# Optimization experiments

Hardware: AMD Instinct MI355X
Metric: run time of the kernel (lower is better)

Reference implementation:

```python
import jax, jax.numpy as jnp
import numpy as np

H = 4            # heads
C = 64           # per-head dim (= hidden, PyG TransformerConv semantics)
HD = 64          # hidden_dim
L = 2            # num_layers
NT = 2           # node types: 0=task, 1=machine
ET = ((0, 1), (1, 0))  # edge types: (src_nt, dst_nt)
N = 16384        # nodes per type (== max_nodes -> simple pos-enc slice)
E = 262144       # edges per edge type


def _ln(x, g, b):
    mu = x.mean(-1, keepdims=True)
    var = ((x - mu) ** 2).mean(-1, keepdims=True)
    return (x - mu) * jax.lax.rsqrt(var + 1e-5) * g + b


def _tconv(x_src, x_dst, ei, Wq, bq, Wk, bk, Wv, bv, Ws, bs, Wb):
    # PyG TransformerConv: heads=H, out_channels=C, concat=False, beta=True
    n_dst = x_dst.shape[0]
    src, dst = ei[0], ei[1]
    q = (x_dst @ Wq + bq).reshape(-1, H, C)
    k = (x_src @ Wk + bk).reshape(-1, H, C)
    v = (x_src @ Wv + bv).reshape(-1, H, C)
    logits = jnp.einsum('ehc,ehc->eh', q[dst], k[src]) * (1.0 / float(np.sqrt(C)))  # [E,H]
    m = jax.ops.segment_max(logits, dst, num_segments=n_dst)          # [N,H] segment softmax
    ex = jnp.exp(logits - m[dst])
    denom = jax.ops.segment_sum(ex, dst, num_segments=n_dst)
    alpha = ex / denom[dst]                                            # [E,H]
    msg = (alpha[:, :, None] * v[src]).reshape(-1, H * C)              # [E,H*C]
    out = jax.ops.segment_sum(msg, dst, num_segments=n_dst)
    out = out.reshape(n_dst, H, C).mean(axis=1)                        # concat=False -> head mean
    r = x_dst @ Ws + bs                                                # lin_skip
    beta = jax.nn.sigmoid(jnp.concatenate([out, r, out - r], -1) @ Wb) # lin_beta, [N,1]
    return beta * r + (1.0 - beta) * out


def _forward(edge_index, x, W_in, b_in, type_emb, pos, Wq, bq, Wk, bk, Wv, bv,
             Wskip, bskip, Wbeta, ln_g, ln_b, ff_W1, ff_b1, ff_W2, ff_b2, W_out, b_out):
    # input proj + type embedding + positional encoding (num_nodes == max_nodes -> slice)
    h = [x[t] @ W_in[t] + b_in[t] + type_emb[t] + pos[t] for t in range(NT)]
    for l in range(L):
        hn = [jnp.zeros_like(h[0]), jnp.zeros_like(h[1])]
        for e, (s, d) in enumerate(ET):  # HeteroConv, aggr='sum'
            hn[d] = hn[d] + _tconv(h[s], h[d], edge_index[e],
                                   Wq[l, e], bq[l, e], Wk[l, e], bk[l, e],
                                   Wv[l, e], bv[l, e], Wskip[l, e], bskip[l, e], Wbeta[l, e])
        for t in range(NT):
            hr = _ln(h[t] + hn[t], ln_g[l, t], ln_b[l, t])
            ff = jax.nn.gelu(hr @ ff_W1[l, t] + ff_b1[l, t], approximate=False) @ ff_W2[l, t] + ff_b2[l, t]
            h[t] = hr + ff
    return jnp.stack([h[t] @ W_out[t] + b_out[t] for t in range(NT)])  # [NT,N,HD]


def setup_inputs() -> dict:
    key = jax.random.key(0)
    ks = jax.random.split(key, 16)
    w = lambda k, s: 0.02 * jax.random.normal(k, s, jnp.float32)
    NE = len(ET)
    return {
        'x': jax.random.normal(ks[0], (NT, N, HD), jnp.float32),
        'edge_index': jax.random.randint(ks[1], (NE, 2, E), 0, N, jnp.int32),
        'W_in': w(ks[2], (NT, HD, HD)), 'b_in': jnp.zeros((NT, HD), jnp.float32),
        'type_emb': w(ks[3], (NT, HD)),
        'pos': w(ks[4], (NT, N, HD)),
        'Wq': w(ks[5], (L, NE, HD, H * C)), 'bq': jnp.zeros((L, NE, H * C), jnp.float32),
        'Wk': w(ks[6], (L, NE, HD, H * C)), 'bk': jnp.zeros((L, NE, H * C), jnp.float32),
        'Wv': w(ks[7], (L, NE, HD, H * C)), 'bv': jnp.zeros((L, NE, H * C), jnp.float32),
        'Wskip': w(ks[8], (L, NE, HD, HD)), 'bskip': jnp.zeros((L, NE, HD), jnp.float32),
        'Wbeta': w(ks[9], (L, NE, 3 * HD, 1)),
        'ln_g': jnp.ones((L, NT, HD), jnp.float32), 'ln_b': jnp.zeros((L, NT, HD), jnp.float32),
        'ff_W1': w(ks[10], (L, NT, HD, 4 * HD)), 'ff_b1': jnp.zeros((L, NT, 4 * HD), jnp.float32),
        'ff_W2': w(ks[11], (L, NT, 4 * HD, HD)), 'ff_b2': jnp.zeros((L, NT, HD), jnp.float32),
        'W_out': w(ks[12], (NT, HD, HD)), 'b_out': jnp.zeros((NT, HD), jnp.float32),
    }


def reference(x, edge_index, W_in, b_in, type_emb, pos, Wq, bq, Wk, bk, Wv, bv,
              Wskip, bskip, Wbeta, ln_g, ln_b, ff_W1, ff_b1, ff_W2, ff_b2, W_out, b_out):
    return _forward(edge_index, x, W_in, b_in, type_emb, pos, Wq, bq, Wk, bk, Wv, bv,
                    Wskip, bskip, Wbeta, ln_g, ln_b, ff_W1, ff_b1, ff_W2, ff_b2, W_out, b_out)
```

## Files before the change

kernel.cpp:

```cpp
#include <hip/hip_runtime.h>
#include <math.h>

#define NN 16384
#define EE 262144

typedef __bf16 v8bf __attribute__((ext_vector_type(8)));
typedef __bf16 v4bf __attribute__((ext_vector_type(4)));
typedef float  v4f  __attribute__((ext_vector_type(4)));
typedef float  v2f  __attribute__((ext_vector_type(2)));

#define OFF_CNT     0
#define OFF_FILL    (2*NN)
#define OFF_ROWPTR  (4*NN)
#define OFF_COLSRC  98816
#define OFF_H       623104
#define OFF_HN      (OFF_H  + 2*NN*64)
#define OFF_Q       (OFF_HN + 2*NN*64)
#define OFF_KV      (OFF_Q  + 2*NN*128)
#define OFF_R       (OFF_KV + 2*NN*192)

__device__ __forceinline__ float blo(unsigned u) { return __uint_as_float(u << 16); }
__device__ __forceinline__ float bhi(unsigned u) { return __uint_as_float(u & 0xffff0000u); }
__device__ __forceinline__ unsigned short f2b(float f) {
  __bf16 h = (__bf16)f;
  return *(unsigned short*)&h;
}

__global__ void count_kernel(const int* __restrict__ ei, int* __restrict__ cnt) {
  int idx = blockIdx.x * 256 + threadIdx.x;
  if (idx >= 2 * EE) return;
  int et = idx >> 18;
  int j  = idx & (EE - 1);
  int dst = ei[et * 2 * EE + EE + j];
  atomicAdd(&cnt[et * NN + dst], 1);
}

__global__ __launch_bounds__(1024) void scan_kernel(const int* __restrict__ cnt,
                                                    int* __restrict__ rowptr,
                                                    int* __restrict__ fill) {
  int et = blockIdx.x;
  const int* c = cnt + et * NN;
  __shared__ int sums[1024];
  int tid = threadIdx.x;
  int base = tid * 16;
  int loc[16];
  int s = 0;
#pragma unroll
  for (int i = 0; i < 16; ++i) { loc[i] = s; s += c[base + i]; }
  sums[tid] = s;
  __syncthreads();
  for (int off = 1; off < 1024; off <<= 1) {
    int v = 0;
    if (tid >= off) v = sums[tid - off];
    __syncthreads();
    if (tid >= off) sums[tid] += v;
    __syncthreads();
  }
  int ebase = (tid == 0) ? 0 : sums[tid - 1];
  int* rp = rowptr + et * (NN + 1);
  int* fl = fill + et * NN;
#pragma unroll
  for (int i = 0; i < 16; ++i) {
    rp[base + i] = ebase + loc[i];
    fl[base + i] = ebase + loc[i];
  }
  if (tid == 1023) rp[NN] = sums[1023];
}

__global__ void scatter_kernel(const int* __restrict__ ei, int* __restrict__ fill,
                               int* __restrict__ colsrc) {
  int idx = blockIdx.x * 256 + threadIdx.x;
  if (idx >= 2 * EE) return;
  int et = idx >> 18;
  int j  = idx & (EE - 1);
  int src = ei[et * 2 * EE + j];
  int dst = ei[et * 2 * EE + EE + j];
  int pos = atomicAdd(&fill[et * NN + dst], 1);
  colsrc[et * EE + pos] = (et * NN + src) * 768;
}

struct GemmDesc {
  const float *A, *B, *bias, *bias2, *add;
  char* C;
  int K, Ncols, Cld, tile0, ntiles, gelu, otype;
};
struct GemmPack { GemmDesc d[8]; int nd; };

#define LDA 72

__global__ __launch_bounds__(256) void gemm_mfma(GemmPack p) {
  int y = blockIdx.y;
  int di = 0;
  for (int i = 0; i < p.nd; ++i)
    if (y >= p.d[i].tile0 && y < p.d[i].tile0 + p.d[i].ntiles) di = i;
  GemmDesc g = p.d[di];
  const int col0 = (y - g.tile0) * 64;
  const int row0 = blockIdx.x * 128;
  const int tid = threadIdx.x;
  const int w = tid >> 6, lane = tid & 63;
  const int l16 = lane & 15, quad = lane >> 4;

  __shared__ __bf16 As[128 * LDA];
  __shared__ __bf16 Bs[64 * LDA];

  v4f acc[2][4];
#pragma unroll
  for (int rt = 0; rt < 2; ++rt)
#pragma unroll
    for (int ct = 0; ct < 4; ++ct)
#pragma unroll
      for (int r = 0; r < 4; ++r) acc[rt][ct][r] = 0.f;

  for (int kt = 0; kt < g.K; kt += 64) {
#pragma unroll
    for (int it = 0; it < 8; ++it) {
      int fi = it * 256 + tid;
      int grow = fi >> 4;
      int kq = (fi & 15) << 2;
      float4 a = *(const float4*)(g.A + (size_t)(row0 + grow) * g.K + kt + kq);
      v4bf c = { (__bf16)a.x, (__bf16)a.y, (__bf16)a.z, (__bf16)a.w };
      *(v4bf*)&As[grow * LDA + kq] = c;
    }
#pragma unroll
    for (int it = 0; it < 4; ++it) {
      int fi = it * 256 + tid;
      int kk = fi >> 4;
      int nq = (fi & 15) << 2;
      float4 b = *(const float4*)(g.B + (size_t)(kt + kk) * g.Ncols + col0 + nq);
      Bs[(nq + 0) * LDA + kk] = (__bf16)b.x;
      Bs[(nq + 1) * LDA + kk] = (__bf16)b.y;
      Bs[(nq + 2) * LDA + kk] = (__bf16)b.z;
      Bs[(nq + 3) * LDA + kk] = (__bf16)b.w;
    }
    __syncthreads();
#pragma unroll
    for (int ks = 0; ks < 2; ++ks) {
      v8bf a0 = *(v8bf*)&As[(w * 32 + l16) * LDA + ks * 32 + quad * 8];
      v8bf a1 = *(v8bf*)&As[(w * 32 + 16 + l16) * LDA + ks * 32 + quad * 8];
#pragma unroll
      for (int ct = 0; ct < 4; ++ct) {
        v8bf bb = *(v8bf*)&Bs[(ct * 16 + l16) * LDA + ks * 32 + quad * 8];
        acc[0][ct] = __builtin_amdgcn_mfma_f32_16x16x32_bf16(a0, bb, acc[0][ct], 0, 0, 0);
        acc[1][ct] = __builtin_amdgcn_mfma_f32_16x16x32_bf16(a1, bb, acc[1][ct], 0, 0, 0);
      }
    }
    __syncthreads();
  }

  float bias_c[4];
#pragma unroll
  for (int ct = 0; ct < 4; ++ct) {
    int col = col0 + ct * 16 + l16;
    float b = g.bias ? g.bias[col] : 0.f;
    if (g.bias2) b += g.bias2[col];
    bias_c[ct] = b;
  }
#pragma unroll
  for (int rt = 0; rt < 2; ++rt)
#pragma unroll
    for (int r = 0; r < 4; ++r) {
      size_t row = row0 + w * 32 + rt * 16 + quad * 4 + r;
      char* cp = g.C + row * (size_t)g.Cld;
#pragma unroll
      for (int ct = 0; ct < 4; ++ct) {
        int col = col0 + ct * 16 + l16;
        float v = acc[rt][ct][r] + bias_c[ct];
        if (g.add) v += g.add[row * g.Ncols + col];
        if (g.gelu) v = 0.5f * v * (1.f + erff(v * 0.70710678118654752f));
        if (g.otype == 0)      *(float*)(cp + col * 4) = v;
        else if (g.otype == 1) *(unsigned short*)(cp + col * 2) = f2b(v);
        else {
          unsigned pk = __builtin_amdgcn_cvt_pk_fp8_f32(v, v, 0, false);
          *(unsigned char*)(cp + col) = (unsigned char)(pk & 0xff);
        }
      }
    }
}

struct FFPack {
  const float *HN, *W1, *b1, *W2, *b2;
  float* H;
};

__global__ __launch_bounds__(256) void ff_fused(FFPack p) {
  const int t = blockIdx.y;
  const int row0 = blockIdx.x * 64;
  const int tid = threadIdx.x;
  const int w = tid >> 6, lane = tid & 63;
  const int l16 = lane & 15, quad = lane >> 4;

  const float* A  = p.HN + ((size_t)t * NN) * 64;
  const float* W1 = p.W1 + (size_t)t * 64 * 256;
  const float* b1 = p.b1 + t * 256;
  const float* W2 = p.W2 + (size_t)t * 256 * 64;
  const float* b2 = p.b2 + t * 64;

  __shared__ __bf16 As[64 * LDA];
  __shared__ __bf16 A2[64 * LDA];
  __shared__ __bf16 B1s[64 * LDA];
  __shared__ __bf16 B2s[64 * LDA];

#pragma unroll
  for (int it = 0; it < 4; ++it) {
    int fi = it * 256 + tid;
    int grow = fi >> 4;
    int kq = (fi & 15) << 2;
    float4 a = *(const float4*)(A + (size_t)(row0 + grow) * 64 + kq);
    v4bf c = { (__bf16)a.x, (__bf16)a.y, (__bf16)a.z, (__bf16)a.w };
    *(v4bf*)&As[grow * LDA + kq] = c;
  }

  v4f acc2[4];
#pragma unroll
  for (int ct = 0; ct < 4; ++ct)
#pragma unroll
    for (int r = 0; r < 4; ++r) acc2[ct][r] = 0.f;

  for (int c1 = 0; c1 < 4; ++c1) {
#pragma unroll
    for (int it = 0; it < 4; ++it) {
      int fi = it * 256 + tid;
      int kk = fi >> 4;
      int nq = (fi & 15) << 2;
      float4 b = *(const float4*)(W1 + (size_t)kk * 256 + c1 * 64 + nq);
      B1s[(nq + 0) * LDA + kk] = (__bf16)b.x;
      B1s[(nq + 1) * LDA + kk] = (__bf16)b.y;
      B1s[(nq + 2) * LDA + kk] = (__bf16)b.z;
      B1s[(nq + 3) * LDA + kk] = (__bf16)b.w;
      float4 b2v = *(const float4*)(W2 + (size_t)(c1 * 64 + kk) * 64 + nq);
      B2s[(nq + 0) * LDA + kk] = (__bf16)b2v.x;
      B2s[(nq + 1) * LDA + kk] = (__bf16)b2v.y;
      B2s[(nq + 2) * LDA + kk] = (__bf16)b2v.z;
      B2s[(nq + 3) * LDA + kk] = (__bf16)b2v.w;
    }
    __syncthreads();

    v4f acc1[4];
#pragma unroll
    for (int ct = 0; ct < 4; ++ct)
#pragma unroll
      for (int r = 0; r < 4; ++r) acc1[ct][r] = 0.f;
#pragma unroll
    for (int ks = 0; ks < 2; ++ks) {
      v8bf a = *(v8bf*)&As[(w * 16 + l16) * LDA + ks * 32 + quad * 8];
#pragma unroll
      for (int ct = 0; ct < 4; ++ct) {
        v8bf bb = *(v8bf*)&B1s[(ct * 16 + l16) * LDA + ks * 32 + quad * 8];
        acc1[ct] = __builtin_amdgcn_mfma_f32_16x16x32_bf16(a, bb, acc1[ct], 0, 0, 0);
      }
    }
#pragma unroll
    for (int ct = 0; ct < 4; ++ct) {
      float bb = b1[c1 * 64 + ct * 16 + l16];
#pragma unroll
      for (int r = 0; r < 4; ++r) {
        float v = acc1[ct][r] + bb;
        v = 0.5f * v * (1.f + erff(v * 0.70710678118654752f));
        A2[(w * 16 + quad * 4 + r) * LDA + ct * 16 + l16] = (__bf16)v;
      }
    }
#pragma unroll
    for (int ks = 0; ks < 2; ++ks) {
      v8bf a = *(v8bf*)&A2[(w * 16 + l16) * LDA + ks * 32 + quad * 8];
#pragma unroll
      for (int ct = 0; ct < 4; ++ct) {
        v8bf bb = *(v8bf*)&B2s[(ct * 16 + l16) * LDA + ks * 32 + quad * 8];
        acc2[ct] = __builtin_amdgcn_mfma_f32_16x16x32_bf16(a, bb, acc2[ct], 0, 0, 0);
      }
    }
    __syncthreads();
  }

#pragma unroll
  for (int ct = 0; ct < 4; ++ct) {
    int col = ct * 16 + l16;
    float bb = b2[col];
#pragma unroll
    for (int r = 0; r < 4; ++r) {
      size_t row = (size_t)t * NN + row0 + w * 16 + quad * 4 + r;
      float v = acc2[ct][r] + bb + p.HN[row * 64 + col];
      p.H[row * 64 + col] = v;
    }
  }
}

struct AggPack {
  const unsigned short *Q;
  const char *KV;
  const float *R;
  const float *Wb;
  const float *Hin;
  const float *lng, *lnb;
  float* outHR;
  const int *rowptr;
  const int *colsrc;
};

__global__ __launch_bounds__(256) void agg_kernel(AggPack p) {
  const int et = blockIdx.y, d = 1 - et;
  int wid = __builtin_amdgcn_readfirstlane(threadIdx.x >> 6);
  int lane = threadIdx.x & 63;
  int node = blockIdx.x * 4 + wid;
  int c4 = lane & 15;
  int cb = ((lane >> 4) << 6) + (c4 << 2);

  const int* rp = p.rowptr + et * (NN + 1);
  const int* cs = p.colsrc + et * EE;
  int start = rp[node], end = rp[node + 1];
  int len = end - start;
  int gnode = d * NN + node;

  uint2 qw = *(const uint2*)(p.Q + ((size_t)gnode << 8) + cb);
  float q0 = blo(qw.x) * 0.125f, q1 = bhi(qw.x) * 0.125f;
  float q2 = blo(qw.y) * 0.125f, q3 = bhi(qw.y) * 0.125f;

  int b[5];
#pragma unroll
  for (int i = 0; i <= 4; ++i) b[i] = start + ((len * i) >> 2);
  float dsum[4] = {0.f, 0.f, 0.f, 0.f};
  float acc[4][4];
#pragma unroll
  for (int s4 = 0; s4 < 4; ++s4)
#pragma unroll
    for (int c = 0; c < 4; ++c) acc[s4][c] = 0.f;

  int maxn = (len + 3) >> 2;
  int last = end - 1;
  for (int it = 0; it < maxn; ++it) {
#pragma unroll
    for (int s4 = 0; s4 < 4; ++s4) {
      int j = b[s4] + it;
      bool act = j < b[s4 + 1];
      int jc = act ? j : last;
      int off = cs[jc];
      const char* rowp = p.KV + off;
      unsigned kw = *(const unsigned*)(rowp + cb);
      uint2 vw = *(const uint2*)(rowp + 256 + cb * 2);
      v2f kl = __builtin_amdgcn_cvt_pk_f32_fp8((int)kw, false);
      v2f kh = __builtin_amdgcn_cvt_pk_f32_fp8((int)kw, true);
      float pd = q0 * kl[0] + q1 * kl[1] + q2 * kh[0] + q3 * kh[1];
      pd += __shfl_xor(pd, 1);
      pd += __shfl_xor(pd, 2);
      pd += __shfl_xor(pd, 4);
      pd += __shfl_xor(pd, 8);
      float wgt = act ? __expf(pd) : 0.f;
      dsum[s4] += wgt;
      acc[s4][0] += wgt * blo(vw.x);
      acc[s4][1] += wgt * bhi(vw.x);
      acc[s4][2] += wgt * blo(vw.y);
      acc[s4][3] += wgt * bhi(vw.y);
    }
  }
  float dn = (dsum[0] + dsum[1]) + (dsum[2] + dsum[3]);
  float ax = (acc[0][0] + acc[1][0]) + (acc[2][0] + acc[3][0]);
  float ay = (acc[0][1] + acc[1][1]) + (acc[2][1] + acc[3][1]);
  float az = (acc[0][2] + acc[1][2]) + (acc[2][2] + acc[3][2]);
  float aw = (acc[0][3] + acc[1][3]) + (acc[2][3] + acc[3][3]);

  float inv = (len > 0) ? (0.25f / dn) : 0.f;
  float ox = ax * inv, oy = ay * inv, oz = az * inv, ow = aw * inv;
  ox += __shfl_xor(ox, 16); ox += __shfl_xor(ox, 32);
  oy += __shfl_xor(oy, 16); oy += __shfl_xor(oy, 32);
  oz += __shfl_xor(oz, 16); oz += __shfl_xor(oz, 32);
  ow += __shfl_xor(ow, 16); ow += __shfl_xor(ow, 32);

  int cc = c4 << 2;
  float4 r = *(const float4*)(p.R + (size_t)gnode * 64 + cc);
  const float* wb = p.Wb + et * 192;
  float part = ox * wb[cc] + oy * wb[cc + 1] + oz * wb[cc + 2] + ow * wb[cc + 3]
             + r.x * wb[64 + cc] + r.y * wb[64 + cc + 1]
             + r.z * wb[64 + cc + 2] + r.w * wb[64 + cc + 3]
             + (ox - r.x) * wb[128 + cc] + (oy - r.y) * wb[128 + cc + 1]
             + (oz - r.z) * wb[128 + cc + 2] + (ow - r.w) * wb[128 + cc + 3];
  part += __shfl_xor(part, 1);
  part += __shfl_xor(part, 2);
  part += __shfl_xor(part, 4);
  part += __shfl_xor(part, 8);
  float beta = 1.f / (1.f + __expf(-part));

  float4 hv = *(const float4*)(p.Hin + (size_t)gnode * 64 + cc);
  float yx = hv.x + beta * r.x + (1.f - beta) * ox;
  float yy = hv.y + beta * r.y + (1.f - beta) * oy;
  float yz = hv.z + beta * r.z + (1.f - beta) * oz;
  float yw = hv.w + beta * r.w + (1.f - beta) * ow;
  float sa = yx + yy + yz + yw;
  float sb = yx * yx + yy * yy + yz * yz + yw * yw;
  sa += __shfl_xor(sa, 1); sb += __shfl_xor(sb, 1);
  sa += __shfl_xor(sa, 2); sb += __shfl_xor(sb, 2);
  sa += __shfl_xor(sa, 4); sb += __shfl_xor(sb, 4);
  sa += __shfl_xor(sa, 8); sb += __shfl_xor(sb, 8);
  float mu = sa * (1.f / 64.f);
  float var = sb * (1.f / 64.f) - mu * mu;
  float rs = rsqrtf(var + 1e-5f);
  if (lane < 16) {
    const float* lng = p.lng + d * 64;
    const float* lnb = p.lnb + d * 64;
    float4 gg = *(const float4*)(lng + cc);
    float4 bb = *(const float4*)(lnb + cc);
    float4 res;
    res.x = (yx - mu) * rs * gg.x + bb.x;
    res.y = (yy - mu) * rs * gg.y + bb.y;
    res.z = (yz - mu) * rs * gg.z + bb.z;
    res.w = (yw - mu) * rs * gg.w + bb.w;
    *(float4*)(p.outHR + (size_t)gnode * 64 + cc) = res;
  }
}

static void add_desc(GemmPack& p, int& tiles, const float* A, const float* B,
                     const float* bias, const float* bias2, const float* add,
                     void* C, int K, int Nc, int Cld, int gelu, int otype) {
  GemmDesc& g = p.d[p.nd++];
  g.A = A; g.B = B; g.bias = bias; g.bias2 = bias2; g.add = add; g.C = (char*)C;
  g.K = K; g.Ncols = Nc; g.Cld = Cld; g.tile0 = tiles; g.ntiles = Nc / 64;
  g.gelu = gelu; g.otype = otype;
  tiles += g.ntiles;
}

extern "C" void kernel_launch(void* const* d_in, const int* in_sizes, int n_in,
                              void* d_out, int out_size, void* d_ws, size_t ws_size,
                              hipStream_t stream) {
  const float* x        = (const float*)d_in[0];
  const int*   ei       = (const int*)d_in[1];
  const float* W_in     = (const float*)d_in[2];
  const float* b_in     = (const float*)d_in[3];
  const float* type_emb = (const float*)d_in[4];
  const float* pos      = (const float*)d_in[5];
  const float* Wq       = (const float*)d_in[6];
  const float* bq       = (const float*)d_in[7];
  const float* Wk       = (const float*)d_in[8];
  const float* bk       = (const float*)d_in[9];
  const float* Wv       = (const float*)d_in[10];
  const float* bv       = (const float*)d_in[11];
  const float* Wskip    = (const float*)d_in[12];
  const float* bskip    = (const float*)d_in[13];
  const float* Wbeta    = (const float*)d_in[14];
  const float* ln_g     = (const float*)d_in[15];
  const float* ln_b     = (const float*)d_in[16];
  const float* ff_W1    = (const float*)d_in[17];
  const float* ff_b1    = (const float*)d_in[18];
  const float* ff_W2    = (const float*)d_in[19];
  const float* ff_b2    = (const float*)d_in[20];
  const float* W_out    = (const float*)d_in[21];
  const float* b_out    = (const float*)d_in[22];
  float* out = (float*)d_out;

  int*   wsi = (int*)d_ws;
  float* wsf = (float*)d_ws;
  int* cnt    = wsi + OFF_CNT;
  int* fill   = wsi + OFF_FILL;
  int* rowptr = wsi + OFF_ROWPTR;
  int* colsrc = wsi + OFF_COLSRC;
  float* H  = wsf + OFF_H;
  float* HN = wsf + OFF_HN;
  unsigned short* Qb = (unsigned short*)(wsf + OFF_Q);
  char* KVb = (char*)(wsf + OFF_KV);
  float* Rb = wsf + OFF_R;

  hipMemsetAsync(cnt, 0, 2 * NN * sizeof(int), stream);
  count_kernel<<<dim3(2 * EE / 256), dim3(256), 0, stream>>>(ei, cnt);
  scan_kernel<<<dim3(2), dim3(1024), 0, stream>>>(cnt, rowptr, fill);
  scatter_kernel<<<dim3(2 * EE / 256), dim3(256), 0, stream>>>(ei, fill, colsrc);

  {
    GemmPack p{}; int tiles = 0;
    for (int t = 0; t < 2; ++t)
      add_desc(p, tiles, x + (size_t)t * NN * 64, W_in + t * 64 * 64,
               b_in + t * 64, type_emb + t * 64, pos + (size_t)t * NN * 64,
               H + (size_t)t * NN * 64, 64, 64, 256, 0, 0);
    gemm_mfma<<<dim3(128, tiles), dim3(256), 0, stream>>>(p);
  }

  for (int l = 0; l < 2; ++l) {
    {
      GemmPack p{}; int tiles = 0;
      for (int et = 0; et < 2; ++et) {
        int s = et, d = 1 - et;
        int we = l * 2 + et;
        const float* hs = H + (size_t)s * NN * 64;
        const float* hd = H + (size_t)d * NN * 64;
        add_desc(p, tiles, hd, Wq + (size_t)we * 64 * 256, bq + we * 256,
                 nullptr, nullptr, (char*)Qb + (size_t)d * NN * 512, 64, 256, 512, 0, 1);
        add_desc(p, tiles, hs, Wk + (size_t)we * 64 * 256, bk + we * 256,
                 nullptr, nullptr, KVb + (size_t)s * NN * 768, 64, 256, 768, 0, 2);
        add_desc(p, tiles, hs, Wv + (size_t)we * 64 * 256, bv + we * 256,
                 nullptr, nullptr, KVb + (size_t)s * NN * 768 + 256, 64, 256, 768, 0, 1);
        add_desc(p, tiles, hd, Wskip + (size_t)we * 64 * 64, bskip + we * 64,
                 nullptr, nullptr, Rb + (size_t)d * NN * 64, 64, 64, 256, 0, 0);
      }
      gemm_mfma<<<dim3(128, tiles), dim3(256), 0, stream>>>(p);
    }

    AggPack ap;
    ap.Q = Qb; ap.KV = KVb; ap.R = Rb;
    ap.Wb = Wbeta + l * 2 * 192;
    ap.Hin = H;
    ap.lng = ln_g + l * 128;
    ap.lnb = ln_b + l * 128;
    ap.outHR = HN;
    ap.rowptr = rowptr;
    ap.colsrc = colsrc;
    agg_kernel<<<dim3(NN / 4, 2), dim3(256), 0, stream>>>(ap);

    FFPack fp;
    fp.HN = HN;
    fp.W1 = ff_W1 + (size_t)l * 2 * 64 * 256;
    fp.b1 = ff_b1 + l * 2 * 256;
    fp.W2 = ff_W2 + (size_t)l * 2 * 256 * 64;
    fp.b2 = ff_b2 + l * 2 * 64;
    fp.H  = H;
    ff_fused<<<dim3(NN / 64, 2), dim3(256), 0, stream>>>(fp);
  }

  {
    GemmPack p{}; int tiles = 0;
    for (int t = 0; t < 2; ++t)
      add_desc(p, tiles, H + (size_t)t * NN * 64, W_out + t * 64 * 64,
               b_out + t * 64, nullptr, nullptr,
               out + (size_t)t * NN * 64, 64, 64, 256, 0, 0);
    gemm_mfma<<<dim3(128, tiles), dim3(256), 0, stream>>>(p);
  }
}
```

Baseline: 394.6 us.

## Fuse QKV/skip projections into input-proj and FFN kernels, drop standalone GEMMs

Removes the generic multi-descriptor GEMM kernel. The input projection now produces H in LDS and immediately computes the Q/K/V/skip projections for layer 0. The FFN kernel of layer 0 does the same for layer 1, and the last FFN computes the output projection. This avoids re-reading H from global memory and saves three kernel launches. In exchange, each block runs many sequential weight loads and syncs over 13 column tiles with a single 64-row tile, which may lower parallelism and occupancy per projection.

```diff
diff --git a/kernel.cpp b/kernel.cpp
--- a/kernel.cpp
+++ b/kernel.cpp
@@ -18,6 +18,8 @@
 #define OFF_Q       (OFF_HN + 2*NN*64)
 #define OFF_KV      (OFF_Q  + 2*NN*128)
 #define OFF_R       (OFF_KV + 2*NN*192)
+
+#define LDA 72
 
 __device__ __forceinline__ float blo(unsigned u) { return __uint_as_float(u << 16); }
 __device__ __forceinline__ float bhi(unsigned u) { return __uint_as_float(u & 0xffff0000u); }
@@ -79,107 +81,158 @@
   colsrc[et * EE + pos] = (et * NN + src) * 768;
 }
 
-struct GemmDesc {
-  const float *A, *B, *bias, *bias2, *add;
-  char* C;
-  int K, Ncols, Cld, tile0, ntiles, gelu, otype;
+struct ProjDesc { const float *B, *bias; char* C; int Ncols, Cld, otype; };
+
+__device__ __forceinline__ void project_from_lds(const __bf16* hA, __bf16* Bs,
+                                                 const ProjDesc* pd, int nd,
+                                                 int row0, int tid) {
+  const int w = tid >> 6, lane = tid & 63;
+  const int l16 = lane & 15, quad = lane >> 4;
+  for (int di = 0; di < nd; ++di) {
+    ProjDesc g = pd[di];
+    for (int ct0 = 0; ct0 < (g.Ncols >> 6); ++ct0) {
+      const int col0 = ct0 * 64;
+      __syncthreads();
+#pragma unroll
+      for (int it = 0; it < 4; ++it) {
+        int fi = it * 256 + tid;
+        int kk = fi >> 4;
+        int nq = (fi & 15) << 2;
+        float4 b = *(const float4*)(g.B + (size_t)kk * g.Ncols + col0 + nq);
+        Bs[(nq + 0) * LDA + kk] = (__bf16)b.x;
+        Bs[(nq + 1) * LDA + kk] = (__bf16)b.y;
+        Bs[(nq + 2) * LDA + kk] = (__bf16)b.z;
+        Bs[(nq + 3) * LDA + kk] = (__bf16)b.w;
+      }
+      __syncthreads();
+
+      v4f acc[4];
+#pragma unroll
+      for (int ct = 0; ct < 4; ++ct)
+#pragma unroll
+        for (int r = 0; r < 4; ++r) acc[ct][r] = 0.f;
+#pragma unroll
+      for (int ks = 0; ks < 2; ++ks) {
+        v8bf a = *(v8bf*)&hA[(w * 16 + l16) * LDA + ks * 32 + quad * 8];
+#pragma unroll
+        for (int ct = 0; ct < 4; ++ct) {
+          v8bf bb = *(v8bf*)&Bs[(ct * 16 + l16) * LDA + ks * 32 + quad * 8];
+          acc[ct] = __builtin_amdgcn_mfma_f32_16x16x32_bf16(a, bb, acc[ct], 0, 0, 0);
+        }
+      }
+#pragma unroll
+      for (int ct = 0; ct < 4; ++ct) {
+        int col = col0 + ct * 16 + l16;
+        float bv = g.bias[col];
+#pragma unroll
+        for (int r = 0; r < 4; ++r) {
+          size_t row = row0 + w * 16 + quad * 4 + r;
+          char* cp = g.C + row * (size_t)g.Cld;
+          float v = acc[ct][r] + bv;
+          if (g.otype == 0)      *(float*)(cp + col * 4) = v;
+          else if (g.otype == 1) *(unsigned short*)(cp + col * 2) = f2b(v);
+          else {
+            unsigned pk = __builtin_amdgcn_cvt_pk_fp8_f32(v, v, 0, false);
+            *(unsigned char*)(cp + col) = (unsigned char)(pk & 0xff);
+          }
+        }
+      }
+    }
+  }
+}
+
+struct InQkvPack {
+  const float *x, *Win, *bin, *temb, *pos;
+  const float *Wq, *bq, *Wk, *bk, *Wv, *bv, *Ws, *bs;
+  float* H;
+  unsigned short* Qb;
+  char* KVb;
+  float* Rb;
 };
-struct GemmPack { GemmDesc d[8]; int nd; };
-
-#define LDA 72
-
-__global__ __launch_bounds__(256) void gemm_mfma(GemmPack p) {
-  int y = blockIdx.y;
-  int di = 0;
-  for (int i = 0; i < p.nd; ++i)
-    if (y >= p.d[i].tile0 && y < p.d[i].tile0 + p.d[i].ntiles) di = i;
-  GemmDesc g = p.d[di];
-  const int col0 = (y - g.tile0) * 64;
-  const int row0 = blockIdx.x * 128;
+
+__global__ __launch_bounds__(256) void in_qkv(InQkvPack p) {
+  const int t = blockIdx.y;
+  const int row0 = blockIdx.x * 64;
   const int tid = threadIdx.x;
   const int w = tid >> 6, lane = tid & 63;
   const int l16 = lane & 15, quad = lane >> 4;
 
-  __shared__ __bf16 As[128 * LDA];
+  __shared__ __bf16 As[64 * LDA];
   __shared__ __bf16 Bs[64 * LDA];
 
-  v4f acc[2][4];
-#pragma unroll
-  for (int rt = 0; rt < 2; ++rt)
-#pragma unroll
-    for (int ct = 0; ct < 4; ++ct)
-#pragma unroll
-      for (int r = 0; r < 4; ++r) acc[rt][ct][r] = 0.f;
-
-  for (int kt = 0; kt < g.K; kt += 64) {
-#pragma unroll
-    for (int it = 0; it < 8; ++it) {
-      int fi = it * 256 + tid;
-      int grow = fi >> 4;
-      int kq = (fi & 15) << 2;
-      float4 a = *(const float4*)(g.A + (size_t)(row0 + grow) * g.K + kt + kq);
-      v4bf c = { (__bf16)a.x, (__bf16)a.y, (__bf16)a.z, (__bf16)a.w };
-      *(v4bf*)&As[grow * LDA + kq] = c;
-    }
-#pragma unroll
-    for (int it = 0; it < 4; ++it) {
-      int fi = it * 256 + tid;
-      int kk = fi >> 4;
-      int nq = (fi & 15) << 2;
-      float4 b = *(const float4*)(g.B + (size_t)(kt + kk) * g.Ncols + col0 + nq);
-      Bs[(nq + 0) * LDA + kk] = (__bf16)b.x;
-      Bs[(nq + 1) * LDA + kk] = (__bf16)b.y;
-      Bs[(nq + 2) * LDA + kk] = (__bf16)b.z;
-      Bs[(nq + 3) * LDA + kk] = (__bf16)b.w;
-    }
-    __syncthreads();
-#pragma unroll
-    for (int ks = 0; ks < 2; ++ks) {
-      v8bf a0 = *(v8bf*)&As[(w * 32 + l16) * LDA + ks * 32 + quad * 8];
-      v8bf a1 = *(v8bf*)&As[(w * 32 + 16 + l16) * LDA + ks * 32 + quad * 8];
-#pragma unroll
-      for (int ct = 0; ct < 4; ++ct) {
-        v8bf bb = *(v8bf*)&Bs[(ct * 16 + l16) * LDA + ks * 32 + quad * 8];
-        acc[0][ct] = __builtin_amdgcn_mfma_f32_16x16x32_bf16(a0, bb, acc[0][ct], 0, 0, 0);
-        acc[1][ct] = __builtin_amdgcn_mfma_f32_16x16x32_bf16(a1, bb, acc[1][ct], 0, 0, 0);
-      }
-    }
-    __syncthreads();
-  }
-
-  float bias_c[4];
+  const float* xs = p.x + ((size_t)t * NN) * 64;
+  const float* Win = p.Win + (size_t)t * 64 * 64;
+
+#pragma unroll
+  for (int it = 0; it < 4; ++it) {
+    int fi = it * 256 + tid;
+    int grow = fi >> 4;
+    int kq = (fi & 15) << 2;
+    float4 a = *(const float4*)(xs + (size_t)(row0 + grow) * 64 + kq);
+    v4bf c = { (__bf16)a.x, (__bf16)a.y, (__bf16)a.z, (__bf16)a.w };
+    *(v4bf*)&As[grow * LDA + kq] = c;
+    int kk = grow, nq = kq;
+    float4 b = *(const float4*)(Win + (size_t)kk * 64 + nq);
+    Bs[(nq + 0) * LDA + kk] = (__bf16)b.x;
+    Bs[(nq + 1) * LDA + kk] = (__bf16)b.y;
+    Bs[(nq + 2) * LDA + kk] = (__bf16)b.z;
+    Bs[(nq + 3) * LDA + kk] = (__bf16)b.w;
+  }
+  __syncthreads();
+
+  v4f acc[4];
+#pragma unroll
+  for (int ct = 0; ct < 4; ++ct)
+#pragma unroll
+    for (int r = 0; r < 4; ++r) acc[ct][r] = 0.f;
+#pragma unroll
+  for (int ks = 0; ks < 2; ++ks) {
+    v8bf a = *(v8bf*)&As[(w * 16 + l16) * LDA + ks * 32 + quad * 8];
+#pragma unroll
+    for (int ct = 0; ct < 4; ++ct) {
+      v8bf bb = *(v8bf*)&Bs[(ct * 16 + l16) * LDA + ks * 32 + quad * 8];
+      acc[ct] = __builtin_amdgcn_mfma_f32_16x16x32_bf16(a, bb, acc[ct], 0, 0, 0);
+    }
+  }
+
+  const float* bin = p.bin + t * 64;
+  const float* temb = p.temb + t * 64;
+  const float* pos = p.pos + ((size_t)t * NN) * 64;
 #pragma unroll
   for (int ct = 0; ct < 4; ++ct) {
-    int col = col0 + ct * 16 + l16;
-    float b = g.bias ? g.bias[col] : 0.f;
-    if (g.bias2) b += g.bias2[col];
-    bias_c[ct] = b;
-  }
-#pragma unroll
-  for (int rt = 0; rt < 2; ++rt)
+    int col = ct * 16 + l16;
+    float bb = bin[col] + temb[col];
 #pragma unroll
     for (int r = 0; r < 4; ++r) {
-      size_t row = row0 + w * 32 + rt * 16 + quad * 4 + r;
-      char* cp = g.C + row * (size_t)g.Cld;
-#pragma unroll
-      for (int ct = 0; ct < 4; ++ct) {
-        int col = col0 + ct * 16 + l16;
-        float v = acc[rt][ct][r] + bias_c[ct];
-        if (g.add) v += g.add[row * g.Ncols + col];
-        if (g.gelu) v = 0.5f * v * (1.f + erff(v * 0.70710678118654752f));
-        if (g.otype == 0)      *(float*)(cp + col * 4) = v;
-        else if (g.otype == 1) *(unsigned short*)(cp + col * 2) = f2b(v);
-        else {
-          unsigned pk = __builtin_amdgcn_cvt_pk_fp8_f32(v, v, 0, false);
-          *(unsigned char*)(cp + col) = (unsigned char)(pk & 0xff);
-        }
-      }
-    }
+      int lrow = w * 16 + quad * 4 + r;
+      size_t row = (size_t)t * NN + row0 + lrow;
+      float v = acc[ct][r] + bb + pos[(size_t)(row0 + lrow) * 64 + col];
+      p.H[row * 64 + col] = v;
+      As[lrow * LDA + col] = (__bf16)v;
+    }
+  }
+
+  int tq = 1 - t;
+  ProjDesc pd[4];
+  pd[0] = { p.Wq + (size_t)tq * 64 * 256, p.bq + tq * 256,
+            (char*)p.Qb + (size_t)t * NN * 512, 256, 512, 1 };
+  pd[1] = { p.Wk + (size_t)t * 64 * 256, p.bk + t * 256,
+            p.KVb + (size_t)t * NN * 768, 256, 768, 2 };
+  pd[2] = { p.Wv + (size_t)t * 64 * 256, p.bv + t * 256,
+            p.KVb + (size_t)t * NN * 768 + 256, 256, 768, 1 };
+  pd[3] = { p.Ws + (size_t)tq * 64 * 64, p.bs + tq * 64,
+            (char*)(p.Rb + (size_t)t * NN * 64), 64, 256, 0 };
+  project_from_lds(As, Bs, pd, 4, row0, tid);
 }
 
 struct FFPack {
   const float *HN, *W1, *b1, *W2, *b2;
   float* H;
+  const float *Wq, *bq, *Wk, *bk, *Wv, *bv, *Ws, *bs;
+  unsigned short* Qb; char* KVb; float* Rb;
+  const float *Wout, *bout;
+  float* outbuf;
+  int mode;
 };
 
 __global__ __launch_bounds__(256) void ff_fused(FFPack p) {
@@ -277,10 +330,31 @@
     float bb = b2[col];
 #pragma unroll
     for (int r = 0; r < 4; ++r) {
-      size_t row = (size_t)t * NN + row0 + w * 16 + quad * 4 + r;
+      int lrow = w * 16 + quad * 4 + r;
+      size_t row = (size_t)t * NN + row0 + lrow;
       float v = acc2[ct][r] + bb + p.HN[row * 64 + col];
-      p.H[row * 64 + col] = v;
-    }
+      if (p.mode == 1) p.H[row * 64 + col] = v;
+      A2[lrow * LDA + col] = (__bf16)v;
+    }
+  }
+
+  if (p.mode == 1) {
+    int tq = 1 - t;
+    ProjDesc pd[4];
+    pd[0] = { p.Wq + (size_t)tq * 64 * 256, p.bq + tq * 256,
+              (char*)p.Qb + (size_t)t * NN * 512, 256, 512, 1 };
+    pd[1] = { p.Wk + (size_t)t * 64 * 256, p.bk + t * 256,
+              p.KVb + (size_t)t * NN * 768, 256, 768, 2 };
+    pd[2] = { p.Wv + (size_t)t * 64 * 256, p.bv + t * 256,
+              p.KVb + (size_t)t * NN * 768 + 256, 256, 768, 1 };
+    pd[3] = { p.Ws + (size_t)tq * 64 * 64, p.bs + tq * 64,
+              (char*)(p.Rb + (size_t)t * NN * 64), 64, 256, 0 };
+    project_from_lds(A2, B1s, pd, 4, row0, tid);
+  } else {
+    ProjDesc pd[1];
+    pd[0] = { p.Wout + (size_t)t * 64 * 64, p.bout + t * 64,
+              (char*)(p.outbuf + (size_t)t * NN * 64), 64, 256, 0 };
+    project_from_lds(A2, B1s, pd, 1, row0, tid);
   }
 }
 
@@ -404,16 +478,6 @@
     res.w = (yw - mu) * rs * gg.w + bb.w;
     *(float4*)(p.outHR + (size_t)gnode * 64 + cc) = res;
   }
-}
-
-static void add_desc(GemmPack& p, int& tiles, const float* A, const float* B,
-                     const float* bias, const float* bias2, const float* add,
-                     void* C, int K, int Nc, int Cld, int gelu, int otype) {
-  GemmDesc& g = p.d[p.nd++];
-  g.A = A; g.B = B; g.bias = bias; g.bias2 = bias2; g.add = add; g.C = (char*)C;
-  g.K = K; g.Ncols = Nc; g.Cld = Cld; g.tile0 = tiles; g.ntiles = Nc / 64;
-  g.gelu = gelu; g.otype = otype;
-  tiles += g.ntiles;
 }
 
 extern "C" void kernel_launch(void* const* d_in, const int* in_sizes, int n_in,
@@ -462,34 +526,15 @@
   scatter_kernel<<<dim3(2 * EE / 256), dim3(256), 0, stream>>>(ei, fill, colsrc);
 
   {
-    GemmPack p{}; int tiles = 0;
-    for (int t = 0; t < 2; ++t)
-      add_desc(p, tiles, x + (size_t)t * NN * 64, W_in + t * 64 * 64,
-               b_in + t * 64, type_emb + t * 64, pos + (size_t)t * NN * 64,
-               H + (size_t)t * NN * 64, 64, 64, 256, 0, 0);
-    gemm_mfma<<<dim3(128, tiles), dim3(256), 0, stream>>>(p);
+    InQkvPack ip;
+    ip.x = x; ip.Win = W_in; ip.bin = b_in; ip.temb = type_emb; ip.pos = pos;
+    ip.Wq = Wq; ip.bq = bq; ip.Wk = Wk; ip.bk = bk;
+    ip.Wv = Wv; ip.bv = bv; ip.Ws = Wskip; ip.bs = bskip;
+    ip.H = H; ip.Qb = Qb; ip.KVb = KVb; ip.Rb = Rb;
+    in_qkv<<<dim3(NN / 64, 2), dim3(256), 0, stream>>>(ip);
   }
 
   for (int l = 0; l < 2; ++l) {
-    {
-      GemmPack p{}; int tiles = 0;
-      for (int et = 0; et < 2; ++et) {
-        int s = et, d = 1 - et;
-        int we = l * 2 + et;
-        const float* hs = H + (size_t)s * NN * 64;
-        const float* hd = H + (size_t)d * NN * 64;
-        add_desc(p, tiles, hd, Wq + (size_t)we * 64 * 256, bq + we * 256,
-                 nullptr, nullptr, (char*)Qb + (size_t)d * NN * 512, 64, 256, 512, 0, 1);
-        add_desc(p, tiles, hs, Wk + (size_t)we * 64 * 256, bk + we * 256,
-                 nullptr, nullptr, KVb + (size_t)s * NN * 768, 64, 256, 768, 0, 2);
-        add_desc(p, tiles, hs, Wv + (size_t)we * 64 * 256, bv + we * 256,
-                 nullptr, nullptr, KVb + (size_t)s * NN * 768 + 256, 64, 256, 768, 0, 1);
-        add_desc(p, tiles, hd, Wskip + (size_t)we * 64 * 64, bskip + we * 64,
-                 nullptr, nullptr, Rb + (size_t)d * NN * 64, 64, 64, 256, 0, 0);
-      }
-      gemm_mfma<<<dim3(128, tiles), dim3(256), 0, stream>>>(p);
-    }
-
     AggPack ap;
     ap.Q = Qb; ap.KV = KVb; ap.R = Rb;
     ap.Wb = Wbeta + l * 2 * 192;
@@ -508,15 +553,21 @@
     fp.W2 = ff_W2 + (size_t)l * 2 * 256 * 64;
     fp.b2 = ff_b2 + l * 2 * 64;
     fp.H  = H;
+    if (l == 0) {
+      fp.mode = 1;
+      fp.Wq = Wq + (size_t)2 * 64 * 256; fp.bq = bq + 2 * 256;
+      fp.Wk = Wk + (size_t)2 * 64 * 256; fp.bk = bk + 2 * 256;
+      fp.Wv = Wv + (size_t)2 * 64 * 256; fp.bv = bv + 2 * 256;
+      fp.Ws = Wskip + (size_t)2 * 64 * 64; fp.bs = bskip + 2 * 64;
+      fp.Qb = Qb; fp.KVb = KVb; fp.Rb = Rb;
+      fp.Wout = nullptr; fp.bout = nullptr; fp.outbuf = nullptr;
+    } else {
+      fp.mode = 2;
+      fp.Wq = fp.Wk = fp.Wv = fp.Ws = nullptr;
+      fp.bq = fp.bk = fp.bv = fp.bs = nullptr;
+      fp.Qb = nullptr; fp.KVb = nullptr; fp.Rb = nullptr;
+      fp.Wout = W_out; fp.bout = b_out; fp.outbuf = out;
+    }
     ff_fused<<<dim3(NN / 64, 2), dim3(256), 0, stream>>>(fp);
   }
-
-  {
-    GemmPack p{}; int tiles = 0;
-    for (int t = 0; t < 2; ++t)
-      add_desc(p, tiles, H + (size_t)t * NN * 64, W_out + t * 64 * 64,
-               b_out + t * 64, nullptr, nullptr,
-               out + (size_t)t * NN * 64, 64, 64, 256, 0, 0);
-    gemm_mfma<<<dim3(128, tiles), dim3(256), 0, stream>>>(p);
-  }
-}
+}
```

After: 428.6 us. 1.09x slower.
